# Performance work log

Hardware: AMD Instinct MI355X
Metric: run time of the kernel (lower is better)

## Reference

```python
import jax, jax.numpy as jnp
import numpy as np


def setup_inputs() -> dict:
    key = jax.random.key(0)
    k1, k2, k3, k4 = jax.random.split(key, 4)
    B, C, D = 128, 1000, 512
    mu = jax.random.normal(k1, (B, D), dtype=jnp.float32)
    std = jax.random.uniform(k2, (B, D), dtype=jnp.float32)
    weight = jax.random.normal(k3, (C, D), dtype=jnp.float32)
    label = jax.random.randint(k4, (B,), 0, C, dtype=jnp.int64)
    return {"mu": mu, "std": std, "weight": weight, "label": label}


def reference(mu, std, weight, label):
    # mu: [B, D], std: [B, D], weight: [C, D], label: [B]
    num_classes = weight.shape[0]
    mu_e = mu[:, None, :].astype(jnp.float32)       # [B, 1, D]
    std_e = std[:, None, :].astype(jnp.float32)     # [B, 1, D]
    dist = jnp.abs(weight[None, :, :] - mu_e)       # [B, C, D]
    y = dist / jnp.sqrt(jnp.float32(2.0)) / (std_e + 1e-8)
    one_hot = jax.nn.one_hot(label, num_classes, dtype=jnp.float32)[..., None]  # [B, C, 1]
    positive = one_hot * y
    negative = (1.0 - one_hot) * y
    erf_value = jax.scipy.special.erf(positive)
    erfc_value = jax.scipy.special.erfc(negative)
    loss = jnp.mean(jnp.sum(erf_value, axis=-1)) + jnp.mean(jnp.sum(erfc_value, axis=-1))
    return loss
```

## Files before the change

kernel.cpp:

```cpp
#include <hip/hip_runtime.h>

#define BB   128
#define CC   1000
#define DD   512
#define CT   8
#define BSPL 16
#define NCT  (CC / CT)
#define NBCH (BB / BSPL)
#define NBLK (NCT * NBCH)

__device__ __forceinline__ float erfc_pos(float x) {
    const float a1 = 0.278393f, a2 = 0.230389f, a3 = 0.000972f, a4 = 0.078108f;
    float p  = fmaf(fmaf(fmaf(fmaf(a4, x, a3), x, a2), x, a1), x, 1.0f);
    float r  = __builtin_amdgcn_rcpf(p);
    float r2 = r * r;
    return r2 * r2;
}

__device__ __forceinline__ float block_reduce(float v) {
    #pragma unroll
    for (int off = 32; off > 0; off >>= 1)
        v += __shfl_down(v, off, 64);
    __shared__ float wsum[4];
    const int lane = threadIdx.x & 63;
    const int wave = threadIdx.x >> 6;
    if (lane == 0) wsum[wave] = v;
    __syncthreads();
    return (wsum[0] + wsum[1]) + (wsum[2] + wsum[3]);
}

__global__ __launch_bounds__(256) void total_kernel(
        const float* __restrict__ mu, const float* __restrict__ sd,
        const float* __restrict__ w, const int* __restrict__ label,
        float* __restrict__ partial) {
    const int ctile = blockIdx.x % NCT;
    const int bchnk = blockIdx.x / NCT;
    const int c0 = ctile * CT;
    const int b0 = bchnk * BSPL;
    const int d0 = threadIdx.x * 2;
    const float rsqrt2 = 0.70710678118654752f;

    float accf = 0.0f;

    if (blockIdx.x < BB) {
        const int b  = blockIdx.x;
        const int lb = label[b];
        float2 wl = *(const float2*)(w + (size_t)lb * DD + d0);
        float2 m  = *(const float2*)(mu + (size_t)b * DD + d0);
        float2 s  = *(const float2*)(sd + (size_t)b * DD + d0);
        float inv0 = rsqrt2 * __builtin_amdgcn_rcpf(s.x + 1e-8f);
        float inv1 = rsqrt2 * __builtin_amdgcn_rcpf(s.y + 1e-8f);
        accf -= 2.0f * (erfc_pos(fabsf(wl.x - m.x) * inv0) +
                        erfc_pos(fabsf(wl.y - m.y) * inv1));
    }

    float2 wv[CT];
    #pragma unroll
    for (int i = 0; i < CT; ++i)
        wv[i] = *(const float2*)(w + (size_t)(c0 + i) * DD + d0);

    for (int bi = 0; bi < BSPL; ++bi) {
        const int b = b0 + bi;
        float2 m = *(const float2*)(mu + (size_t)b * DD + d0);
        float2 s = *(const float2*)(sd + (size_t)b * DD + d0);
        float inv0 = rsqrt2 * __builtin_amdgcn_rcpf(s.x + 1e-8f);
        float inv1 = rsqrt2 * __builtin_amdgcn_rcpf(s.y + 1e-8f);
        #pragma unroll
        for (int i = 0; i < CT; ++i) {
            accf += erfc_pos(fabsf(wv[i].x - m.x) * inv0);
            accf += erfc_pos(fabsf(wv[i].y - m.y) * inv1);
        }
    }

    float s = block_reduce(accf);
    if (threadIdx.x == 0) partial[blockIdx.x] = s;
}

__global__ __launch_bounds__(256) void finalize_kernel(
        const float* __restrict__ partial, float* __restrict__ out) {
    double s = 0.0;
    for (int i = threadIdx.x; i < NBLK; i += 256)
        s += (double)partial[i];
    #pragma unroll
    for (int off = 32; off > 0; off >>= 1)
        s += __shfl_down(s, off, 64);
    __shared__ double dsum[4];
    const int lane = threadIdx.x & 63;
    const int wave = threadIdx.x >> 6;
    if (lane == 0) dsum[wave] = s;
    __syncthreads();
    if (threadIdx.x == 0) {
        double total = (dsum[0] + dsum[1]) + (dsum[2] + dsum[3]);
        out[0] = (float)((2.0 * BB * DD + total) / (double)(BB * CC));
    }
}

extern "C" void kernel_launch(void* const* d_in, const int* in_sizes, int n_in,
                              void* d_out, int out_size, void* d_ws, size_t ws_size,
                              hipStream_t stream) {
    const float* mu    = (const float*)d_in[0];
    const float* sd    = (const float*)d_in[1];
    const float* w     = (const float*)d_in[2];
    const int*   label = (const int*)d_in[3];
    float* out     = (float*)d_out;
    float* partial = (float*)d_ws;

    total_kernel<<<dim3(NBLK), dim3(256), 0, stream>>>(mu, sd, w, label, partial);
    finalize_kernel<<<dim3(1), dim3(256), 0, stream>>>(partial, out);
}
```

Baseline: 84.75 us.

## Split classes across thread halves with float4 loads and prefetch next batch row

Each block's two 128-thread halves now take four classes each, and every thread covers four D elements through float4 loads. The batch chunk per block is halved, which doubles the grid to 2000 blocks. The next mu/std row is prefetched in software and two accumulators are used to lengthen dependency chains. The aim is fewer load instructions, more parallelism and hidden load latency, at the cost of loading mu/std twice as often overall and writing more partials.

```diff
diff --git a/kernel.cpp b/kernel.cpp
--- a/kernel.cpp
+++ b/kernel.cpp
@@ -4,7 +4,7 @@
 #define CC   1000
 #define DD   512
 #define CT   8
-#define BSPL 16
+#define BSPL 8
 #define NCT  (CC / CT)
 #define NBCH (BB / BSPL)
 #define NBLK (NCT * NBCH)
@@ -29,51 +29,65 @@
     return (wsum[0] + wsum[1]) + (wsum[2] + wsum[3]);
 }
 
-__global__ __launch_bounds__(256) void total_kernel(
+__global__ __launch_bounds__(256) void erf_main(
         const float* __restrict__ mu, const float* __restrict__ sd,
         const float* __restrict__ w, const int* __restrict__ label,
         float* __restrict__ partial) {
     const int ctile = blockIdx.x % NCT;
-    const int bchnk = blockIdx.x / NCT;
-    const int c0 = ctile * CT;
-    const int b0 = bchnk * BSPL;
-    const int d0 = threadIdx.x * 2;
+    const int bch   = blockIdx.x / NCT;
+    const int g     = threadIdx.x >> 7;
+    const int dl    = threadIdx.x & 127;
+    const int d0    = dl * 4;
+    const int c0    = ctile * CT + g * 4;
+    const int b0    = bch * BSPL;
     const float rsqrt2 = 0.70710678118654752f;
 
-    float accf = 0.0f;
+    float acc0 = 0.0f, acc1 = 0.0f;
 
-    if (blockIdx.x < BB) {
+    if (blockIdx.x < BB && g == 0) {
         const int b  = blockIdx.x;
         const int lb = label[b];
-        float2 wl = *(const float2*)(w + (size_t)lb * DD + d0);
-        float2 m  = *(const float2*)(mu + (size_t)b * DD + d0);
-        float2 s  = *(const float2*)(sd + (size_t)b * DD + d0);
-        float inv0 = rsqrt2 * __builtin_amdgcn_rcpf(s.x + 1e-8f);
-        float inv1 = rsqrt2 * __builtin_amdgcn_rcpf(s.y + 1e-8f);
-        accf -= 2.0f * (erfc_pos(fabsf(wl.x - m.x) * inv0) +
-                        erfc_pos(fabsf(wl.y - m.y) * inv1));
+        float4 wl = *(const float4*)(w  + (size_t)lb * DD + d0);
+        float4 m  = *(const float4*)(mu + (size_t)b  * DD + d0);
+        float4 s  = *(const float4*)(sd + (size_t)b  * DD + d0);
+        float i0 = rsqrt2 * __builtin_amdgcn_rcpf(s.x + 1e-8f);
+        float i1 = rsqrt2 * __builtin_amdgcn_rcpf(s.y + 1e-8f);
+        float i2 = rsqrt2 * __builtin_amdgcn_rcpf(s.z + 1e-8f);
+        float i3 = rsqrt2 * __builtin_amdgcn_rcpf(s.w + 1e-8f);
+        acc0 -= 2.0f * (erfc_pos(fabsf(wl.x - m.x) * i0) +
+                        erfc_pos(fabsf(wl.y - m.y) * i1));
+        acc1 -= 2.0f * (erfc_pos(fabsf(wl.z - m.z) * i2) +
+                        erfc_pos(fabsf(wl.w - m.w) * i3));
     }
 
-    float2 wv[CT];
+    float4 wv[4];
     #pragma unroll
-    for (int i = 0; i < CT; ++i)
-        wv[i] = *(const float2*)(w + (size_t)(c0 + i) * DD + d0);
+    for (int i = 0; i < 4; ++i)
+        wv[i] = *(const float4*)(w + (size_t)(c0 + i) * DD + d0);
 
+    float4 m = *(const float4*)(mu + (size_t)b0 * DD + d0);
+    float4 s = *(const float4*)(sd + (size_t)b0 * DD + d0);
     for (int bi = 0; bi < BSPL; ++bi) {
-        const int b = b0 + bi;
-        float2 m = *(const float2*)(mu + (size_t)b * DD + d0);
-        float2 s = *(const float2*)(sd + (size_t)b * DD + d0);
-        float inv0 = rsqrt2 * __builtin_amdgcn_rcpf(s.x + 1e-8f);
-        float inv1 = rsqrt2 * __builtin_amdgcn_rcpf(s.y + 1e-8f);
+        const int bn = b0 + (bi + 1 < BSPL ? bi + 1 : bi);
+        float4 mn = *(const float4*)(mu + (size_t)bn * DD + d0);
+        float4 sn = *(const float4*)(sd + (size_t)bn * DD + d0);
+
+        float i0 = rsqrt2 * __builtin_amdgcn_rcpf(s.x + 1e-8f);
+        float i1 = rsqrt2 * __builtin_amdgcn_rcpf(s.y + 1e-8f);
+        float i2 = rsqrt2 * __builtin_amdgcn_rcpf(s.z + 1e-8f);
+        float i3 = rsqrt2 * __builtin_amdgcn_rcpf(s.w + 1e-8f);
         #pragma unroll
-        for (int i = 0; i < CT; ++i) {
-            accf += erfc_pos(fabsf(wv[i].x - m.x) * inv0);
-            accf += erfc_pos(fabsf(wv[i].y - m.y) * inv1);
+        for (int i = 0; i < 4; ++i) {
+            acc0 += erfc_pos(fabsf(wv[i].x - m.x) * i0);
+            acc1 += erfc_pos(fabsf(wv[i].y - m.y) * i1);
+            acc0 += erfc_pos(fabsf(wv[i].z - m.z) * i2);
+            acc1 += erfc_pos(fabsf(wv[i].w - m.w) * i3);
         }
+        m = mn; s = sn;
     }
 
-    float s = block_reduce(accf);
-    if (threadIdx.x == 0) partial[blockIdx.x] = s;
+    float ssum = block_reduce(acc0 + acc1);
+    if (threadIdx.x == 0) partial[blockIdx.x] = ssum;
 }
 
 __global__ __launch_bounds__(256) void finalize_kernel(
@@ -105,6 +119,6 @@
     float* out     = (float*)d_out;
     float* partial = (float*)d_ws;
 
-    total_kernel<<<dim3(NBLK), dim3(256), 0, stream>>>(mu, sd, w, label, partial);
+    erf_main<<<dim3(NBLK), dim3(256), 0, stream>>>(mu, sd, w, label, partial);
     finalize_kernel<<<dim3(1), dim3(256), 0, stream>>>(partial, out);
 }
```

After: 84.53 us. Within noise of the previous version (-0.3%).
